# Kernel optimization log

Measured on AMD Instinct MI355X. Metric: run time of the kernel, lower is better.

## Reference

```python
import jax, jax.numpy as jnp
import numpy as np

N_NODES = 100000
N_EDGES = 1600000
IN_DIM, HIDDEN, OUT = 128, 64, 32


def setup_inputs() -> dict:
    key = jax.random.key(0)
    k1, k2, k3, k4 = jax.random.split(key, 4)
    x = jax.random.normal(k1, (N_NODES, IN_DIM), dtype=jnp.float32)
    edge_index = jax.random.randint(k2, (2, N_EDGES), 0, N_NODES, dtype=jnp.int64)
    # Glorot-style init for GCN weights
    W1 = jax.random.normal(k3, (IN_DIM, HIDDEN), dtype=jnp.float32) / np.sqrt(IN_DIM)
    b1 = jnp.zeros((HIDDEN,), dtype=jnp.float32)
    W2 = jax.random.normal(k4, (HIDDEN, OUT), dtype=jnp.float32) / np.sqrt(HIDDEN)
    b2 = jnp.zeros((OUT,), dtype=jnp.float32)
    return {"x": x, "edge_index": edge_index, "W1": W1, "b1": b1, "W2": W2, "b2": b2}


def _gcn_conv(x, src, dst, W, b, n_nodes):
    """PyG GCNConv: h = W x; symmetric-normalized scatter-add over edges
    (self-loops already appended to src/dst)."""
    h = x @ W  # [N, F_out] — transform first (F_out <= F_in)
    ones = jnp.ones_like(dst, dtype=h.dtype)
    deg = jax.ops.segment_sum(ones, dst, num_segments=n_nodes)  # in-degree incl. self-loop
    dinv = jnp.where(deg > 0, jax.lax.rsqrt(deg), 0.0)
    norm = dinv[src] * dinv[dst]  # [E]
    msg = h[src] * norm[:, None]  # [E, F_out] — dominant gather
    agg = jax.ops.segment_sum(msg, dst, num_segments=n_nodes)  # [N, F_out]
    return agg + b


def reference(x, edge_index, W1, b1, W2, b2):
    n_nodes = x.shape[0]
    loops = jnp.arange(n_nodes, dtype=edge_index.dtype)
    src = jnp.concatenate([edge_index[0], loops])
    dst = jnp.concatenate([edge_index[1], loops])
    h = jax.nn.relu(_gcn_conv(x, src, dst, W1, b1, n_nodes))
    out = jax.nn.relu(_gcn_conv(h, src, dst, W2, b2, n_nodes))
    return out
```

## Files before the change

### kernel.cpp

```cpp
#include <hip/hip_runtime.h>

#define IN_DIM 128
#define HID    64
#define OUTD   32

#define BSHIFT 9
#define BNODES 512
#define NB     196
#define BCAP   16384
#define CHUNK  4096

#define XPAD   136

typedef __attribute__((ext_vector_type(8))) short bf16x8;
typedef __attribute__((ext_vector_type(4))) float f32x4;


__device__ __forceinline__ unsigned bfp2(float x, float y) {
    unsigned a = __float_as_uint(x); a = a + 0x7FFF + ((a >> 16) & 1);
    unsigned b = __float_as_uint(y); b = b + 0x7FFF + ((b >> 16) & 1);
    return (a >> 16) | (b & 0xFFFF0000u);
}

__device__ __forceinline__ unsigned short bf1(float x) {
    unsigned u = __float_as_uint(x);
    u += 0x7FFF + ((u >> 16) & 1);
    return (unsigned short)(u >> 16);
}

__device__ __forceinline__ void acc8(float* f, uint4 q) {
    f[0] += __uint_as_float(q.x << 16); f[1] += __uint_as_float(q.x & 0xFFFF0000u);
    f[2] += __uint_as_float(q.y << 16); f[3] += __uint_as_float(q.y & 0xFFFF0000u);
    f[4] += __uint_as_float(q.z << 16); f[5] += __uint_as_float(q.z & 0xFFFF0000u);
    f[6] += __uint_as_float(q.w << 16); f[7] += __uint_as_float(q.w & 0xFFFF0000u);
}


__global__ void k_binit(int* __restrict__ bucketCursor) {
    int t = threadIdx.x;
    if (t < NB) bucketCursor[t] = t * BCAP;
}


__launch_bounds__(256)
__global__ void k_bscatter(const int* __restrict__ src, const int* __restrict__ dst,
                           int* __restrict__ bucketCursor, int* __restrict__ ebuf, int E) {
    __shared__ int h[NB];
    __shared__ int lbase[NB];
    __shared__ int lcur[NB];
    const int t = threadIdx.x;
    const int base = blockIdx.x * CHUNK;
    const int nI4 = (min(CHUNK, E - base)) >> 2;
    const int4* d4 = (const int4*)(dst + base);
    const int4* s4 = (const int4*)(src + base);

    int4 dv0, dv1, dv2, dv3;
    const bool v0 = t < nI4, v1 = t + 256 < nI4, v2 = t + 512 < nI4, v3 = t + 768 < nI4;
    if (v0) dv0 = d4[t];
    if (v1) dv1 = d4[t + 256];
    if (v2) dv2 = d4[t + 512];
    if (v3) dv3 = d4[t + 768];

    for (int i = t; i < NB; i += 256) { h[i] = 0; lcur[i] = 0; }
    __syncthreads();

    if (v0) { atomicAdd(&h[dv0.x >> BSHIFT], 1); atomicAdd(&h[dv0.y >> BSHIFT], 1);
              atomicAdd(&h[dv0.z >> BSHIFT], 1); atomicAdd(&h[dv0.w >> BSHIFT], 1); }
    if (v1) { atomicAdd(&h[dv1.x >> BSHIFT], 1); atomicAdd(&h[dv1.y >> BSHIFT], 1);
              atomicAdd(&h[dv1.z >> BSHIFT], 1); atomicAdd(&h[dv1.w >> BSHIFT], 1); }
    if (v2) { atomicAdd(&h[dv2.x >> BSHIFT], 1); atomicAdd(&h[dv2.y >> BSHIFT], 1);
              atomicAdd(&h[dv2.z >> BSHIFT], 1); atomicAdd(&h[dv2.w >> BSHIFT], 1); }
    if (v3) { atomicAdd(&h[dv3.x >> BSHIFT], 1); atomicAdd(&h[dv3.y >> BSHIFT], 1);
              atomicAdd(&h[dv3.z >> BSHIFT], 1); atomicAdd(&h[dv3.w >> BSHIFT], 1); }
    __syncthreads();

    for (int i = t; i < NB; i += 256)
        lbase[i] = h[i] ? atomicAdd(&bucketCursor[i], h[i]) : 0;
    __syncthreads();

    #define SC1(D, S) { int b_ = (D) >> BSHIFT; int off_ = atomicAdd(&lcur[b_], 1); \
                        ebuf[lbase[b_] + off_] = ((S) << BSHIFT) | ((D) & (BNODES - 1)); }
    if (v0) { int4 sv = s4[t];       SC1(dv0.x, sv.x); SC1(dv0.y, sv.y); SC1(dv0.z, sv.z); SC1(dv0.w, sv.w); }
    if (v1) { int4 sv = s4[t + 256]; SC1(dv1.x, sv.x); SC1(dv1.y, sv.y); SC1(dv1.z, sv.z); SC1(dv1.w, sv.w); }
    if (v2) { int4 sv = s4[t + 512]; SC1(dv2.x, sv.x); SC1(dv2.y, sv.y); SC1(dv2.z, sv.z); SC1(dv2.w, sv.w); }
    if (v3) { int4 sv = s4[t + 768]; SC1(dv3.x, sv.x); SC1(dv3.y, sv.y); SC1(dv3.z, sv.z); SC1(dv3.w, sv.w); }
    #undef SC1
}


__launch_bounds__(256)
__global__ void k_bfinal(const int* __restrict__ ebuf, const int* __restrict__ bucketCursor,
                         int* __restrict__ rs, int* __restrict__ re, float* __restrict__ dinv,
                         int* __restrict__ csr, int N) {
    __shared__ int hist[BNODES];
    __shared__ int rsl[BNODES];
    __shared__ int ssum[256];
    const int t = threadIdx.x;
    const int b = blockIdx.x;
    const int nodeBase = b << BSHIFT;
    const int ebase = b * BCAP;
    const int cnt = bucketCursor[b] - ebase;
    const int nI4 = cnt >> 2;
    const int4* e4 = (const int4*)(ebuf + ebase);

    hist[t] = 0; hist[t + 256] = 0;
    __syncthreads();
    for (int i = t; i < nI4; i += 256) {
        int4 v = e4[i];
        atomicAdd(&hist[v.x & (BNODES - 1)], 1);
        atomicAdd(&hist[v.y & (BNODES - 1)], 1);
        atomicAdd(&hist[v.z & (BNODES - 1)], 1);
        atomicAdd(&hist[v.w & (BNODES - 1)], 1);
    }
    if (t < (cnt & 3))
        atomicAdd(&hist[ebuf[ebase + (nI4 << 2) + t] & (BNODES - 1)], 1);
    __syncthreads();

    int h0 = hist[2 * t], h1 = hist[2 * t + 1];
    ssum[t] = h0 + h1;
    __syncthreads();
    for (int off = 1; off < 256; off <<= 1) {
        int u = (t >= off) ? ssum[t - off] : 0;
        __syncthreads();
        ssum[t] += u;
        __syncthreads();
    }
    int excl = ssum[t] - h0 - h1;
    rsl[2 * t]     = excl;
    rsl[2 * t + 1] = excl + h0;

    int n0 = nodeBase + 2 * t, n1 = n0 + 1;
    if (n0 < N) {
        rs[n0] = ebase + excl;           re[n0] = ebase + excl + h0;
        dinv[n0] = rsqrtf((float)h0 + 1.0f);
    }
    if (n1 < N) {
        rs[n1] = ebase + excl + h0;      re[n1] = ebase + excl + h0 + h1;
        dinv[n1] = rsqrtf((float)h1 + 1.0f);
    }

    hist[2 * t] = 0; hist[2 * t + 1] = 0;
    __syncthreads();

    #define FILL1(P) { int l_ = (P) & (BNODES - 1); int off_ = atomicAdd(&hist[l_], 1); \
                       csr[ebase + rsl[l_] + off_] = ((unsigned)(P)) >> BSHIFT; }
    for (int i = t; i < nI4; i += 256) {
        int4 v = e4[i];
        FILL1(v.x); FILL1(v.y); FILL1(v.z); FILL1(v.w);
    }
    if (t < (cnt & 3))
        FILL1(ebuf[ebase + (nI4 << 2) + t]);
    #undef FILL1
}


__launch_bounds__(256)
__global__ void k_gemm1(const float* __restrict__ x, const float* __restrict__ W1,
                        const float* __restrict__ dinv, unsigned short* __restrict__ hs1b, int N) {
    __shared__ unsigned short xsb[64 * XPAD];
    __shared__ unsigned short wsb[64 * XPAD];
    const int t = threadIdx.x;
    const int base = blockIdx.x * 64;

    for (int i = t; i < IN_DIM * HID; i += 256) {
        int k = i >> 6, n = i & 63;
        wsb[n * XPAD + k] = bf1(W1[i]);
    }
    {
        const float4* s4 = (const float4*)(x + (size_t)base * IN_DIM);
        #pragma unroll
        for (int j = 0; j < 8; ++j) {
            int idx = t + j * 256;
            int r = idx >> 5, k4 = (idx & 31) * 4;
            ushort4 o;
            if (base + r < N) {
                float4 v = s4[idx];
                o.x = bf1(v.x); o.y = bf1(v.y); o.z = bf1(v.z); o.w = bf1(v.w);
            } else {
                o.x = 0; o.y = 0; o.z = 0; o.w = 0;
            }
            *(ushort4*)&xsb[r * XPAD + k4] = o;
        }
    }
    __syncthreads();

    const int lane = t & 63;
    const int w    = t >> 6;
    const int lr   = lane & 15;
    const int kg   = lane >> 4;

    f32x4 acc0 = {0,0,0,0}, acc1 = {0,0,0,0}, acc2 = {0,0,0,0}, acc3 = {0,0,0,0};
    #pragma unroll
    for (int kb = 0; kb < 4; ++kb) {
        int ko = kb * 32 + kg * 8;
        bf16x8 af = *(const bf16x8*)&xsb[(w * 16 + lr) * XPAD + ko];
        bf16x8 b0 = *(const bf16x8*)&wsb[( 0 + lr) * XPAD + ko];
        bf16x8 b1 = *(const bf16x8*)&wsb[(16 + lr) * XPAD + ko];
        bf16x8 b2 = *(const bf16x8*)&wsb[(32 + lr) * XPAD + ko];
        bf16x8 b3 = *(const bf16x8*)&wsb[(48 + lr) * XPAD + ko];
        acc0 = __builtin_amdgcn_mfma_f32_16x16x32_bf16(af, b0, acc0, 0, 0, 0);
        acc1 = __builtin_amdgcn_mfma_f32_16x16x32_bf16(af, b1, acc1, 0, 0, 0);
        acc2 = __builtin_amdgcn_mfma_f32_16x16x32_bf16(af, b2, acc2, 0, 0, 0);
        acc3 = __builtin_amdgcn_mfma_f32_16x16x32_bf16(af, b3, acc3, 0, 0, 0);
    }

    #pragma unroll
    for (int j = 0; j < 4; ++j) {
        int node = base + w * 16 + kg * 4 + j;
        if (node < N) {
            float d = dinv[node];
            unsigned short* o = hs1b + (size_t)node * HID + lr;
            o[0]  = bf1(acc0[j] * d);
            o[16] = bf1(acc1[j] * d);
            o[32] = bf1(acc2[j] * d);
            o[48] = bf1(acc3[j] * d);
        }
    }
}


__launch_bounds__(256)
__global__ void k_fuse2(const uint4* __restrict__ hs, const int* __restrict__ rs,
                        const int* __restrict__ re, const int* __restrict__ csr,
                        const float* __restrict__ dinv,
                        const float* __restrict__ b1, const float* __restrict__ W2,
                        uint2* __restrict__ hs2b, int N) {
    __shared__ float Ws[HID * OUTD];
    __shared__ float L1s[32 * 68];
    const int t = threadIdx.x;
    const int base = blockIdx.x * 32;

    for (int i = t; i < HID * OUTD / 4; i += 256)
        ((float4*)Ws)[i] = ((const float4*)W2)[i];

    {
        int node = base + (t >> 3);
        int lane = t & 7;
        float fa[8] = {0,0,0,0,0,0,0,0};
        float fb[8] = {0,0,0,0,0,0,0,0};
        float fc[8] = {0,0,0,0,0,0,0,0};
        float fd[8] = {0,0,0,0,0,0,0,0};
        if (node < N) {
            acc8(fa, hs[(size_t)node * 8 + lane]);
            int i = rs[node], end = re[node];
            int lim = i + ((end - i) & ~3);
            if (i < lim) {
                int s0 = __builtin_nontemporal_load(csr + i);
                int s1 = __builtin_nontemporal_load(csr + i + 1);
                int s2 = __builtin_nontemporal_load(csr + i + 2);
                int s3 = __builtin_nontemporal_load(csr + i + 3);
                for (i += 4; i < lim; i += 4) {
                    uint4 q0 = hs[(size_t)s0 * 8 + lane];
                    uint4 q1 = hs[(size_t)s1 * 8 + lane];
                    uint4 q2 = hs[(size_t)s2 * 8 + lane];
                    uint4 q3 = hs[(size_t)s3 * 8 + lane];
                    s0 = __builtin_nontemporal_load(csr + i);
                    s1 = __builtin_nontemporal_load(csr + i + 1);
                    s2 = __builtin_nontemporal_load(csr + i + 2);
                    s3 = __builtin_nontemporal_load(csr + i + 3);
                    acc8(fa, q0); acc8(fb, q1); acc8(fc, q2); acc8(fd, q3);
                }
                uint4 q0 = hs[(size_t)s0 * 8 + lane];
                uint4 q1 = hs[(size_t)s1 * 8 + lane];
                uint4 q2 = hs[(size_t)s2 * 8 + lane];
                uint4 q3 = hs[(size_t)s3 * 8 + lane];
                acc8(fa, q0); acc8(fb, q1); acc8(fc, q2); acc8(fd, q3);
            }
            for (; lim < end; ++lim) {
                int s = __builtin_nontemporal_load(csr + lim);
                acc8(fa, hs[(size_t)s * 8 + lane]);
            }
            float dn = dinv[node];
            const float4* bb4 = (const float4*)(b1 + lane * 8);
            float4 bv0 = bb4[0], bv1 = bb4[1];
            float* Lrow = &L1s[(t >> 3) * 68 + lane * 8];
            Lrow[0] = fmaxf((fa[0] + fb[0] + fc[0] + fd[0]) * dn + bv0.x, 0.0f);
            Lrow[1] = fmaxf((fa[1] + fb[1] + fc[1] + fd[1]) * dn + bv0.y, 0.0f);
            Lrow[2] = fmaxf((fa[2] + fb[2] + fc[2] + fd[2]) * dn + bv0.z, 0.0f);
            Lrow[3] = fmaxf((fa[3] + fb[3] + fc[3] + fd[3]) * dn + bv0.w, 0.0f);
            Lrow[4] = fmaxf((fa[4] + fb[4] + fc[4] + fd[4]) * dn + bv1.x, 0.0f);
            Lrow[5] = fmaxf((fa[5] + fb[5] + fc[5] + fd[5]) * dn + bv1.y, 0.0f);
            Lrow[6] = fmaxf((fa[6] + fb[6] + fc[6] + fd[6]) * dn + bv1.z, 0.0f);
            Lrow[7] = fmaxf((fa[7] + fb[7] + fc[7] + fd[7]) * dn + bv1.w, 0.0f);
        } else {
            float* Lrow = &L1s[(t >> 3) * 68 + lane * 8];
            #pragma unroll
            for (int j = 0; j < 8; ++j) Lrow[j] = 0.0f;
        }
    }
    __syncthreads();

    {
        const int fq = t & 7;
        const int nl = t >> 3;
        float4 a = {0,0,0,0};
        #pragma unroll 8
        for (int k = 0; k < HID; ++k) {
            float4 w = ((const float4*)Ws)[k * 8 + fq];
            float xv = L1s[nl * 68 + k];
            a.x += xv * w.x; a.y += xv * w.y; a.z += xv * w.z; a.w += xv * w.w;
        }
        int n = base + nl;
        if (n < N) {
            float d = dinv[n];
            a.x *= d; a.y *= d; a.z *= d; a.w *= d;
            hs2b[(size_t)n * 8 + fq] = make_uint2(bfp2(a.x, a.y), bfp2(a.z, a.w));
        }
    }
}


__launch_bounds__(256)
__global__ void k_agg2(const uint4* __restrict__ hs, const int* __restrict__ rs,
                       const int* __restrict__ re, const int* __restrict__ csr,
                       const float* __restrict__ dinv,
                       const float* __restrict__ b2, float* __restrict__ out, int N) {
    int tid = blockIdx.x * 256 + threadIdx.x;
    int node = tid >> 2;
    if (node >= N) return;
    int lane = tid & 3;

    float fa[8] = {0,0,0,0,0,0,0,0};
    float fb[8] = {0,0,0,0,0,0,0,0};
    float fc[8] = {0,0,0,0,0,0,0,0};
    float fd[8] = {0,0,0,0,0,0,0,0};
    acc8(fa, hs[(size_t)node * 4 + lane]);
    int i = rs[node], end = re[node];
    int lim = i + ((end - i) & ~3);
    if (i < lim) {
        int s0 = __builtin_nontemporal_load(csr + i);
        int s1 = __builtin_nontemporal_load(csr + i + 1);
        int s2 = __builtin_nontemporal_load(csr + i + 2);
        int s3 = __builtin_nontemporal_load(csr + i + 3);
        for (i += 4; i < lim; i += 4) {
            uint4 q0 = hs[(size_t)s0 * 4 + lane];
            uint4 q1 = hs[(size_t)s1 * 4 + lane];
            uint4 q2 = hs[(size_t)s2 * 4 + lane];
            uint4 q3 = hs[(size_t)s3 * 4 + lane];
            s0 = __builtin_nontemporal_load(csr + i);
            s1 = __builtin_nontemporal_load(csr + i + 1);
            s2 = __builtin_nontemporal_load(csr + i + 2);
            s3 = __builtin_nontemporal_load(csr + i + 3);
            acc8(fa, q0); acc8(fb, q1); acc8(fc, q2); acc8(fd, q3);
        }
        uint4 q0 = hs[(size_t)s0 * 4 + lane];
        uint4 q1 = hs[(size_t)s1 * 4 + lane];
        uint4 q2 = hs[(size_t)s2 * 4 + lane];
        uint4 q3 = hs[(size_t)s3 * 4 + lane];
        acc8(fa, q0); acc8(fb, q1); acc8(fc, q2); acc8(fd, q3);
    }
    for (; lim < end; ++lim) {
        int s = __builtin_nontemporal_load(csr + lim);
        acc8(fa, hs[(size_t)s * 4 + lane]);
    }
    float dn = dinv[node];
    const float4* bb4 = (const float4*)(b2 + lane * 8);
    float4 b0 = bb4[0], b1v = bb4[1];
    float4 o0, o1;
    o0.x = fmaxf((fa[0] + fb[0] + fc[0] + fd[0]) * dn + b0.x, 0.0f);
    o0.y = fmaxf((fa[1] + fb[1] + fc[1] + fd[1]) * dn + b0.y, 0.0f);
    o0.z = fmaxf((fa[2] + fb[2] + fc[2] + fd[2]) * dn + b0.z, 0.0f);
    o0.w = fmaxf((fa[3] + fb[3] + fc[3] + fd[3]) * dn + b0.w, 0.0f);
    o1.x = fmaxf((fa[4] + fb[4] + fc[4] + fd[4]) * dn + b1v.x, 0.0f);
    o1.y = fmaxf((fa[5] + fb[5] + fc[5] + fd[5]) * dn + b1v.y, 0.0f);
    o1.z = fmaxf((fa[6] + fb[6] + fc[6] + fd[6]) * dn + b1v.z, 0.0f);
    o1.w = fmaxf((fa[7] + fb[7] + fc[7] + fd[7]) * dn + b1v.w, 0.0f);
    float4* o = (float4*)(out + (size_t)node * OUTD + lane * 8);
    o[0] = o0;
    o[1] = o1;
}


extern "C" void kernel_launch(void* const* d_in, const int* in_sizes, int n_in,
                              void* d_out, int out_size, void* d_ws, size_t ws_size,
                              hipStream_t stream) {
    const float* x  = (const float*)d_in[0];
    const int*   ei = (const int*)  d_in[1];
    const float* W1 = (const float*)d_in[2];
    const float* b1 = (const float*)d_in[3];
    const float* W2 = (const float*)d_in[4];
    const float* b2 = (const float*)d_in[5];

    const int N = in_sizes[0] / IN_DIM;
    const int E = in_sizes[1] / 2;
    const int* srcI = ei;
    const int* dstI = ei + E;
    float* out = (float*)d_out;

    float* dinv         = (float*)d_ws;
    int*   rs           = (int*)d_ws + 131072;
    int*   re           = (int*)d_ws + 2 * 131072;
    int*   bucketCursor = (int*)d_ws + 3 * 131072;
    int*   ebuf         = (int*)d_ws + 4 * 131072;
    int*   csr          = ebuf + (size_t)NB * BCAP;
    uint2* hs1b         = (uint2*)(csr + (size_t)NB * BCAP);
    uint2* hs2b         = hs1b + (size_t)N * 16;

    k_binit   <<<1, 256, 0, stream>>>(bucketCursor);
    k_bscatter<<<(E + CHUNK - 1) / CHUNK, 256, 0, stream>>>(srcI, dstI, bucketCursor, ebuf, E);
    k_bfinal  <<<NB, 256, 0, stream>>>(ebuf, bucketCursor, rs, re, dinv, csr, N);

    k_gemm1<<<(N + 63) / 64, 256, 0, stream>>>(x, W1, dinv, (unsigned short*)hs1b, N);
    k_fuse2<<<(N + 31) / 32, 256, 0, stream>>>((const uint4*)hs1b, rs, re, csr, dinv, b1, W2, hs2b, N);
    k_agg2 <<<(N * 4 + 255) / 256, 256, 0, stream>>>((const uint4*)hs2b, rs, re, csr, dinv, b2, out, N);
}
```

Before: 132.0 us.

## Use persistent work-stealing blocks with atomic group counters for aggregation kernels

Converts k_fuse2 and k_agg2 from one-block-per-tile grids into persistent grids of 2048 blocks that pull 32- or 64-node groups from atomic counters initialised in k_binit. The aim is to cut block launch and scheduling overhead and to balance uneven per-node degrees. It also replaces the software-pipelined index prefetch with a simpler 4/2/1 unrolled loop. In exchange it adds an atomic and extra barriers per group, and it hardcodes the group counts G1CNT and G2CNT for N=100000.

```diff
diff --git a/kernel.cpp b/kernel.cpp
--- a/kernel.cpp
+++ b/kernel.cpp
@@ -12,6 +12,10 @@
 
 #define XPAD   136
 
+#define G1CNT  3125
+#define G2CNT  1563
+#define WSGRID 2048
+
 typedef __attribute__((ext_vector_type(8))) short bf16x8;
 typedef __attribute__((ext_vector_type(4))) float f32x4;
 
@@ -39,6 +43,8 @@
 __global__ void k_binit(int* __restrict__ bucketCursor) {
     int t = threadIdx.x;
     if (t < NB) bucketCursor[t] = t * BCAP;
+    if (t == NB)     bucketCursor[NB] = 0;
+    if (t == NB + 1) bucketCursor[NB + 1] = 0;
 }
 
 
@@ -224,150 +230,164 @@
                         const int* __restrict__ re, const int* __restrict__ csr,
                         const float* __restrict__ dinv,
                         const float* __restrict__ b1, const float* __restrict__ W2,
-                        uint2* __restrict__ hs2b, int N) {
+                        uint2* __restrict__ hs2b, int* __restrict__ wcount, int N) {
     __shared__ float Ws[HID * OUTD];
     __shared__ float L1s[32 * 68];
+    __shared__ int grpS;
     const int t = threadIdx.x;
-    const int base = blockIdx.x * 32;
 
     for (int i = t; i < HID * OUTD / 4; i += 256)
         ((float4*)Ws)[i] = ((const float4*)W2)[i];
 
-    {
-        int node = base + (t >> 3);
-        int lane = t & 7;
-        float fa[8] = {0,0,0,0,0,0,0,0};
-        float fb[8] = {0,0,0,0,0,0,0,0};
-        float fc[8] = {0,0,0,0,0,0,0,0};
-        float fd[8] = {0,0,0,0,0,0,0,0};
+    while (true) {
+        if (t == 0) grpS = atomicAdd(wcount, 1);
+        __syncthreads();
+        const int grp = grpS;
+        if (grp >= G1CNT) break;
+        const int base = grp * 32;
+
+        {
+            int node = base + (t >> 3);
+            int lane = t & 7;
+            float fa[8] = {0,0,0,0,0,0,0,0};
+            float fb[8] = {0,0,0,0,0,0,0,0};
+            float fc[8] = {0,0,0,0,0,0,0,0};
+            float fd[8] = {0,0,0,0,0,0,0,0};
+            if (node < N) {
+                acc8(fa, hs[(size_t)node * 8 + lane]);
+                int i = rs[node];
+                const int end = re[node];
+                for (; i + 4 <= end; i += 4) {
+                    int s0 = __builtin_nontemporal_load(csr + i);
+                    int s1 = __builtin_nontemporal_load(csr + i + 1);
+                    int s2 = __builtin_nontemporal_load(csr + i + 2);
+                    int s3 = __builtin_nontemporal_load(csr + i + 3);
+                    uint4 q0 = hs[(size_t)s0 * 8 + lane];
+                    uint4 q1 = hs[(size_t)s1 * 8 + lane];
+                    uint4 q2 = hs[(size_t)s2 * 8 + lane];
+                    uint4 q3 = hs[(size_t)s3 * 8 + lane];
+                    acc8(fa, q0); acc8(fb, q1); acc8(fc, q2); acc8(fd, q3);
+                }
+                if (i + 2 <= end) {
+                    int s0 = __builtin_nontemporal_load(csr + i);
+                    int s1 = __builtin_nontemporal_load(csr + i + 1);
+                    uint4 q0 = hs[(size_t)s0 * 8 + lane];
+                    uint4 q1 = hs[(size_t)s1 * 8 + lane];
+                    acc8(fa, q0); acc8(fb, q1);
+                    i += 2;
+                }
+                if (i < end) {
+                    int s0 = __builtin_nontemporal_load(csr + i);
+                    acc8(fa, hs[(size_t)s0 * 8 + lane]);
+                }
+                float dn = dinv[node];
+                const float4* bb4 = (const float4*)(b1 + lane * 8);
+                float4 bv0 = bb4[0], bv1 = bb4[1];
+                float* Lrow = &L1s[(t >> 3) * 68 + lane * 8];
+                Lrow[0] = fmaxf((fa[0] + fb[0] + fc[0] + fd[0]) * dn + bv0.x, 0.0f);
+                Lrow[1] = fmaxf((fa[1] + fb[1] + fc[1] + fd[1]) * dn + bv0.y, 0.0f);
+                Lrow[2] = fmaxf((fa[2] + fb[2] + fc[2] + fd[2]) * dn + bv0.z, 0.0f);
+                Lrow[3] = fmaxf((fa[3] + fb[3] + fc[3] + fd[3]) * dn + bv0.w, 0.0f);
+                Lrow[4] = fmaxf((fa[4] + fb[4] + fc[4] + fd[4]) * dn + bv1.x, 0.0f);
+                Lrow[5] = fmaxf((fa[5] + fb[5] + fc[5] + fd[5]) * dn + bv1.y, 0.0f);
+                Lrow[6] = fmaxf((fa[6] + fb[6] + fc[6] + fd[6]) * dn + bv1.z, 0.0f);
+                Lrow[7] = fmaxf((fa[7] + fb[7] + fc[7] + fd[7]) * dn + bv1.w, 0.0f);
+            } else {
+                float* Lrow = &L1s[(t >> 3) * 68 + lane * 8];
+                #pragma unroll
+                for (int j = 0; j < 8; ++j) Lrow[j] = 0.0f;
+            }
+        }
+        __syncthreads();
+
+        {
+            const int fq = t & 7;
+            const int nl = t >> 3;
+            float4 a = {0,0,0,0};
+            #pragma unroll 8
+            for (int k = 0; k < HID; ++k) {
+                float4 w = ((const float4*)Ws)[k * 8 + fq];
+                float xv = L1s[nl * 68 + k];
+                a.x += xv * w.x; a.y += xv * w.y; a.z += xv * w.z; a.w += xv * w.w;
+            }
+            int n = base + nl;
+            if (n < N) {
+                float d = dinv[n];
+                a.x *= d; a.y *= d; a.z *= d; a.w *= d;
+                hs2b[(size_t)n * 8 + fq] = make_uint2(bfp2(a.x, a.y), bfp2(a.z, a.w));
+            }
+        }
+        __syncthreads();
+    }
+}
+
+
+__launch_bounds__(256)
+__global__ void k_agg2(const uint4* __restrict__ hs, const int* __restrict__ rs,
+                       const int* __restrict__ re, const int* __restrict__ csr,
+                       const float* __restrict__ dinv,
+                       const float* __restrict__ b2, float* __restrict__ out,
+                       int* __restrict__ wcount, int N) {
+    __shared__ int grpS;
+    const int t = threadIdx.x;
+    const int lane = t & 3;
+
+    while (true) {
+        if (t == 0) grpS = atomicAdd(wcount, 1);
+        __syncthreads();
+        const int grp = grpS;
+        if (grp >= G2CNT) break;
+        const int node = grp * 64 + (t >> 2);
+
         if (node < N) {
-            acc8(fa, hs[(size_t)node * 8 + lane]);
-            int i = rs[node], end = re[node];
-            int lim = i + ((end - i) & ~3);
-            if (i < lim) {
+            float fa[8] = {0,0,0,0,0,0,0,0};
+            float fb[8] = {0,0,0,0,0,0,0,0};
+            float fc[8] = {0,0,0,0,0,0,0,0};
+            float fd[8] = {0,0,0,0,0,0,0,0};
+            acc8(fa, hs[(size_t)node * 4 + lane]);
+            int i = rs[node];
+            const int end = re[node];
+            for (; i + 4 <= end; i += 4) {
                 int s0 = __builtin_nontemporal_load(csr + i);
                 int s1 = __builtin_nontemporal_load(csr + i + 1);
                 int s2 = __builtin_nontemporal_load(csr + i + 2);
                 int s3 = __builtin_nontemporal_load(csr + i + 3);
-                for (i += 4; i < lim; i += 4) {
-                    uint4 q0 = hs[(size_t)s0 * 8 + lane];
-                    uint4 q1 = hs[(size_t)s1 * 8 + lane];
-                    uint4 q2 = hs[(size_t)s2 * 8 + lane];
-                    uint4 q3 = hs[(size_t)s3 * 8 + lane];
-                    s0 = __builtin_nontemporal_load(csr + i);
-                    s1 = __builtin_nontemporal_load(csr + i + 1);
-                    s2 = __builtin_nontemporal_load(csr + i + 2);
-                    s3 = __builtin_nontemporal_load(csr + i + 3);
-                    acc8(fa, q0); acc8(fb, q1); acc8(fc, q2); acc8(fd, q3);
-                }
-                uint4 q0 = hs[(size_t)s0 * 8 + lane];
-                uint4 q1 = hs[(size_t)s1 * 8 + lane];
-                uint4 q2 = hs[(size_t)s2 * 8 + lane];
-                uint4 q3 = hs[(size_t)s3 * 8 + lane];
+                uint4 q0 = hs[(size_t)s0 * 4 + lane];
+                uint4 q1 = hs[(size_t)s1 * 4 + lane];
+                uint4 q2 = hs[(size_t)s2 * 4 + lane];
+                uint4 q3 = hs[(size_t)s3 * 4 + lane];
                 acc8(fa, q0); acc8(fb, q1); acc8(fc, q2); acc8(fd, q3);
             }
-            for (; lim < end; ++lim) {
-                int s = __builtin_nontemporal_load(csr + lim);
-                acc8(fa, hs[(size_t)s * 8 + lane]);
+            if (i + 2 <= end) {
+                int s0 = __builtin_nontemporal_load(csr + i);
+                int s1 = __builtin_nontemporal_load(csr + i + 1);
+                uint4 q0 = hs[(size_t)s0 * 4 + lane];
+                uint4 q1 = hs[(size_t)s1 * 4 + lane];
+                acc8(fa, q0); acc8(fb, q1);
+                i += 2;
+            }
+            if (i < end) {
+                int s0 = __builtin_nontemporal_load(csr + i);
+                acc8(fa, hs[(size_t)s0 * 4 + lane]);
             }
             float dn = dinv[node];
-            const float4* bb4 = (const float4*)(b1 + lane * 8);
-            float4 bv0 = bb4[0], bv1 = bb4[1];
-            float* Lrow = &L1s[(t >> 3) * 68 + lane * 8];
-            Lrow[0] = fmaxf((fa[0] + fb[0] + fc[0] + fd[0]) * dn + bv0.x, 0.0f);
-            Lrow[1] = fmaxf((fa[1] + fb[1] + fc[1] + fd[1]) * dn + bv0.y, 0.0f);
-            Lrow[2] = fmaxf((fa[2] + fb[2] + fc[2] + fd[2]) * dn + bv0.z, 0.0f);
-            Lrow[3] = fmaxf((fa[3] + fb[3] + fc[3] + fd[3]) * dn + bv0.w, 0.0f);
-            Lrow[4] = fmaxf((fa[4] + fb[4] + fc[4] + fd[4]) * dn + bv1.x, 0.0f);
-            Lrow[5] = fmaxf((fa[5] + fb[5] + fc[5] + fd[5]) * dn + bv1.y, 0.0f);
-            Lrow[6] = fmaxf((fa[6] + fb[6] + fc[6] + fd[6]) * dn + bv1.z, 0.0f);
-            Lrow[7] = fmaxf((fa[7] + fb[7] + fc[7] + fd[7]) * dn + bv1.w, 0.0f);
-        } else {
-            float* Lrow = &L1s[(t >> 3) * 68 + lane * 8];
-            #pragma unroll
-            for (int j = 0; j < 8; ++j) Lrow[j] = 0.0f;
+            const float4* bb4 = (const float4*)(b2 + lane * 8);
+            float4 b0 = bb4[0], b1v = bb4[1];
+            float4 o0, o1;
+            o0.x = fmaxf((fa[0] + fb[0] + fc[0] + fd[0]) * dn + b0.x, 0.0f);
+            o0.y = fmaxf((fa[1] + fb[1] + fc[1] + fd[1]) * dn + b0.y, 0.0f);
+            o0.z = fmaxf((fa[2] + fb[2] + fc[2] + fd[2]) * dn + b0.z, 0.0f);
+            o0.w = fmaxf((fa[3] + fb[3] + fc[3] + fd[3]) * dn + b0.w, 0.0f);
+            o1.x = fmaxf((fa[4] + fb[4] + fc[4] + fd[4]) * dn + b1v.x, 0.0f);
+            o1.y = fmaxf((fa[5] + fb[5] + fc[5] + fd[5]) * dn + b1v.y, 0.0f);
+            o1.z = fmaxf((fa[6] + fb[6] + fc[6] + fd[6]) * dn + b1v.z, 0.0f);
+            o1.w = fmaxf((fa[7] + fb[7] + fc[7] + fd[7]) * dn + b1v.w, 0.0f);
+            float4* o = (float4*)(out + (size_t)node * OUTD + lane * 8);
+            o[0] = o0;
+            o[1] = o1;
         }
-    }
-    __syncthreads();
-
-    {
-        const int fq = t & 7;
-        const int nl = t >> 3;
-        float4 a = {0,0,0,0};
-        #pragma unroll 8
-        for (int k = 0; k < HID; ++k) {
-            float4 w = ((const float4*)Ws)[k * 8 + fq];
-            float xv = L1s[nl * 68 + k];
-            a.x += xv * w.x; a.y += xv * w.y; a.z += xv * w.z; a.w += xv * w.w;
-        }
-        int n = base + nl;
-        if (n < N) {
-            float d = dinv[n];
-            a.x *= d; a.y *= d; a.z *= d; a.w *= d;
-            hs2b[(size_t)n * 8 + fq] = make_uint2(bfp2(a.x, a.y), bfp2(a.z, a.w));
-        }
-    }
-}
-
-
-__launch_bounds__(256)
-__global__ void k_agg2(const uint4* __restrict__ hs, const int* __restrict__ rs,
-                       const int* __restrict__ re, const int* __restrict__ csr,
-                       const float* __restrict__ dinv,
-                       const float* __restrict__ b2, float* __restrict__ out, int N) {
-    int tid = blockIdx.x * 256 + threadIdx.x;
-    int node = tid >> 2;
-    if (node >= N) return;
-    int lane = tid & 3;
-
-    float fa[8] = {0,0,0,0,0,0,0,0};
-    float fb[8] = {0,0,0,0,0,0,0,0};
-    float fc[8] = {0,0,0,0,0,0,0,0};
-    float fd[8] = {0,0,0,0,0,0,0,0};
-    acc8(fa, hs[(size_t)node * 4 + lane]);
-    int i = rs[node], end = re[node];
-    int lim = i + ((end - i) & ~3);
-    if (i < lim) {
-        int s0 = __builtin_nontemporal_load(csr + i);
-        int s1 = __builtin_nontemporal_load(csr + i + 1);
-        int s2 = __builtin_nontemporal_load(csr + i + 2);
-        int s3 = __builtin_nontemporal_load(csr + i + 3);
-        for (i += 4; i < lim; i += 4) {
-            uint4 q0 = hs[(size_t)s0 * 4 + lane];
-            uint4 q1 = hs[(size_t)s1 * 4 + lane];
-            uint4 q2 = hs[(size_t)s2 * 4 + lane];
-            uint4 q3 = hs[(size_t)s3 * 4 + lane];
-            s0 = __builtin_nontemporal_load(csr + i);
-            s1 = __builtin_nontemporal_load(csr + i + 1);
-            s2 = __builtin_nontemporal_load(csr + i + 2);
-            s3 = __builtin_nontemporal_load(csr + i + 3);
-            acc8(fa, q0); acc8(fb, q1); acc8(fc, q2); acc8(fd, q3);
-        }
-        uint4 q0 = hs[(size_t)s0 * 4 + lane];
-        uint4 q1 = hs[(size_t)s1 * 4 + lane];
-        uint4 q2 = hs[(size_t)s2 * 4 + lane];
-        uint4 q3 = hs[(size_t)s3 * 4 + lane];
-        acc8(fa, q0); acc8(fb, q1); acc8(fc, q2); acc8(fd, q3);
-    }
-    for (; lim < end; ++lim) {
-        int s = __builtin_nontemporal_load(csr + lim);
-        acc8(fa, hs[(size_t)s * 4 + lane]);
-    }
-    float dn = dinv[node];
-    const float4* bb4 = (const float4*)(b2 + lane * 8);
-    float4 b0 = bb4[0], b1v = bb4[1];
-    float4 o0, o1;
-    o0.x = fmaxf((fa[0] + fb[0] + fc[0] + fd[0]) * dn + b0.x, 0.0f);
-    o0.y = fmaxf((fa[1] + fb[1] + fc[1] + fd[1]) * dn + b0.y, 0.0f);
-    o0.z = fmaxf((fa[2] + fb[2] + fc[2] + fd[2]) * dn + b0.z, 0.0f);
-    o0.w = fmaxf((fa[3] + fb[3] + fc[3] + fd[3]) * dn + b0.w, 0.0f);
-    o1.x = fmaxf((fa[4] + fb[4] + fc[4] + fd[4]) * dn + b1v.x, 0.0f);
-    o1.y = fmaxf((fa[5] + fb[5] + fc[5] + fd[5]) * dn + b1v.y, 0.0f);
-    o1.z = fmaxf((fa[6] + fb[6] + fc[6] + fd[6]) * dn + b1v.z, 0.0f);
-    o1.w = fmaxf((fa[7] + fb[7] + fc[7] + fd[7]) * dn + b1v.w, 0.0f);
-    float4* o = (float4*)(out + (size_t)node * OUTD + lane * 8);
-    o[0] = o0;
-    o[1] = o1;
+        __syncthreads();
+    }
 }
 
 
@@ -395,12 +415,14 @@
     int*   csr          = ebuf + (size_t)NB * BCAP;
     uint2* hs1b         = (uint2*)(csr + (size_t)NB * BCAP);
     uint2* hs2b         = hs1b + (size_t)N * 16;
+    int*   wc1          = bucketCursor + NB;
+    int*   wc2          = bucketCursor + NB + 1;
 
     k_binit   <<<1, 256, 0, stream>>>(bucketCursor);
     k_bscatter<<<(E + CHUNK - 1) / CHUNK, 256, 0, stream>>>(srcI, dstI, bucketCursor, ebuf, E);
     k_bfinal  <<<NB, 256, 0, stream>>>(ebuf, bucketCursor, rs, re, dinv, csr, N);
 
     k_gemm1<<<(N + 63) / 64, 256, 0, stream>>>(x, W1, dinv, (unsigned short*)hs1b, N);
-    k_fuse2<<<(N + 31) / 32, 256, 0, stream>>>((const uint4*)hs1b, rs, re, csr, dinv, b1, W2, hs2b, N);
-    k_agg2 <<<(N * 4 + 255) / 256, 256, 0, stream>>>((const uint4*)hs2b, rs, re, csr, dinv, b2, out, N);
-}
+    k_fuse2<<<WSGRID, 256, 0, stream>>>((const uint4*)hs1b, rs, re, csr, dinv, b1, W2, hs2b, wc1, N);
+    k_agg2 <<<WSGRID, 256, 0, stream>>>((const uint4*)hs2b, rs, re, csr, dinv, b2, out, wc2, N);
+}
```

Result: slower. 199.6 us (+51.1%).
